# Performance work log

Hardware: AMD Instinct MI355X
Metric: run time of the kernel (lower is better)

Reference implementation:

```python
import jax, jax.numpy as jnp
from jax import lax
import numpy as np

B, N, F = 256, 131072, 16


def _fir(x, h):
    """y[i] = x[i] + sum_{j=0}^{F-1} h[j] * x[i-j-1] for i >= F, else 0.

    x: (B, N) float, h: (F,) float. Implemented as one causal conv with an
    effective (F+1)-tap kernel k where k[0] = 1 (identity) and k[1:] = h.
    """
    f = h.shape[0]
    k = jnp.concatenate([jnp.ones((1,), dtype=h.dtype), h])          # (F+1,)
    # XLA conv is cross-correlation: out[i] = sum_d rhs[d] * lhs_pad[i+d].
    # With left-pad f and a reversed kernel, out[i] = sum_d k[d] * x[i-d].
    out = lax.conv_general_dilated(
        x[:, None, :],                        # (B, 1, N)
        k[::-1][None, None, :],               # (1, 1, F+1)
        window_strides=(1,),
        padding=[(f, 0)],
        dimension_numbers=("NCH", "OIH", "NCH"),
    )[:, 0, :]                                # (B, N)
    # Original code leaves y[i] = 0 for i < F.
    mask = jnp.arange(x.shape[-1]) >= f       # (N,)
    return jnp.where(mask, out, jnp.zeros((), dtype=x.dtype))


def setup_inputs() -> dict:
    key = jax.random.key(0)
    k1, k2 = jax.random.split(key)
    x = jax.random.normal(k1, (B, N), dtype=jnp.float32)
    # keras 'random_normal' initializer: stddev = 0.05
    kernel = jax.random.normal(k2, (1, F), dtype=jnp.float32) * 0.05
    return {"x": x, "kernel": kernel}


def reference(x, kernel):
    h = kernel[0]              # (F,) forward taps
    hr = h[::-1]               # reversed kernel (self.kernel_r)
    v = _fir(x, h)             # first deconv pass with kernel
    y = _fir(v, hr)            # second deconv pass with reversed kernel
    return y
```

## Files before the change

### kernel.cpp

```cpp
#include <hip/hip_runtime.h>


#define NROW 131072
#define TILE 4096
#define HALO 32
#define PADIDX(j) ((j) + ((((j) >> 5)) << 2))
#define LDS_FLOATS (PADIDX(TILE + HALO - 1) + 1)

typedef float f32x4 __attribute__((ext_vector_type(4)));

__global__ void compute_g_kernel(const float* __restrict__ h, float* __restrict__ g) {
    int m = threadIdx.x;
    if (m < 33) {
        float s = 0.f;
#pragma unroll
        for (int a = 0; a <= 16; ++a) {
            int b = m - a;
            if (b >= 0 && b <= 16) {
                float ka = (a == 0) ? 1.f : h[a - 1];
                float kb = (b == 0) ? 1.f : h[16 - b];
                s += ka * kb;
            }
        }
        g[m] = s;
    }
}

__global__ __launch_bounds__(256) void fir2_kernel(const float* __restrict__ x,
                                                   const float* __restrict__ g,
                                                   const float* __restrict__ h,
                                                   float* __restrict__ y) {
    __shared__ __align__(16) float lds[LDS_FLOATS];

    const int bid = blockIdx.x;
    const int row = bid >> 5;
    const int chunk = bid & 31;
    const int i0 = chunk * TILE;
    const int t = (int)threadIdx.x;
    const float* __restrict__ xr = x + (size_t)row * NROW;
    float* __restrict__ yr = y + (size_t)row * NROW;

    float gg[33];
#pragma unroll
    for (int m = 0; m < 33; ++m) gg[m] = g[m];

    const int base = i0 - HALO;
#pragma unroll
    for (int k = 0; k < 4; ++k) {
        const int f = t + 256 * k;
        const int gidx = base + 4 * f;
        f32x4 v = (f32x4)(0.f);
        if (gidx >= 0) v = *(const f32x4*)(xr + gidx);
        *(f32x4*)(lds + PADIDX(4 * f)) = v;
    }
    if (t < 8) {
        const int f = 1024 + t;
        f32x4 v = *(const f32x4*)(xr + base + 4 * f);
        *(f32x4*)(lds + PADIDX(4 * f)) = v;
    }
    __syncthreads();

#pragma unroll 1
    for (int k = 0; k < 4; ++k) {
        const int jb = 1024 * k + 4 * t;
        float w[36];
#pragma unroll
        for (int q = 0; q < 9; ++q) {
            const f32x4 v = *(const f32x4*)(lds + PADIDX(jb + 4 * q));
            w[4 * q + 0] = v.x; w[4 * q + 1] = v.y;
            w[4 * q + 2] = v.z; w[4 * q + 3] = v.w;
        }
        f32x4 o;
#pragma unroll
        for (int c = 0; c < 4; ++c) {
            float s = 0.f;
#pragma unroll
            for (int m = 0; m < 33; ++m) s = fmaf(gg[m], w[c + 32 - m], s);
            o[c] = s;
        }
        __builtin_nontemporal_store(o, (f32x4*)(yr + i0 + jb));
    }

    if (chunk == 0 && t < 8) {
        f32x4 o = (f32x4)(0.f);
        if (t >= 4) {
            float hh[16];
#pragma unroll
            for (int j = 0; j < 16; ++j) hh[j] = h[j];
            float vloc[16];
#pragma unroll
            for (int u = 0; u < 16; ++u) {
                const int p = 16 + u;
                float s = lds[PADIDX(p + 32)];
#pragma unroll
                for (int j = 0; j < 16; ++j)
                    s = fmaf(hh[j], lds[PADIDX(p + 31 - j)], s);
                vloc[u] = s;
            }
#pragma unroll
            for (int p = 16; p < 32; ++p) {
                float s = vloc[p - 16];
#pragma unroll
                for (int j = 0; j < 16; ++j)
                    if (j <= p - 17) s = fmaf(hh[15 - j], vloc[p - 17 - j], s);
                if ((p >> 2) == t) o[p & 3] = s;
            }
        }
        __builtin_nontemporal_store(o, (f32x4*)(yr + 4 * t));
    }
}

extern "C" void kernel_launch(void* const* d_in, const int* in_sizes, int n_in,
                              void* d_out, int out_size, void* d_ws, size_t ws_size,
                              hipStream_t stream) {
    const float* x = (const float*)d_in[0];
    const float* h = (const float*)d_in[1];
    float* y = (float*)d_out;
    float* g = (float*)d_ws;
    (void)in_sizes; (void)n_in; (void)out_size; (void)ws_size;

    compute_g_kernel<<<1, 64, 0, stream>>>(h, g);
    fir2_kernel<<<8192, 256, 0, stream>>>(x, g, h, y);
}
```

Baseline: 236.9 us.

## Drop LDS staging and read FIR windows directly from global memory

Removes the shared-memory tile and barrier. Each thread now loads its 36-sample window straight from global memory and computes one 4-output group. The grid grows fourfold so each block covers a quarter of the previous tile. Overlapping window reads now rely on L1/L2 caching instead of explicit LDS reuse, which trades extra global load traffic for no sync and no LDS occupancy limit.

```diff
diff --git a/kernel.cpp b/kernel.cpp
--- a/kernel.cpp
+++ b/kernel.cpp
@@ -2,10 +2,6 @@
 
 
 #define NROW 131072
-#define TILE 4096
-#define HALO 32
-#define PADIDX(j) ((j) + ((((j) >> 5)) << 2))
-#define LDS_FLOATS (PADIDX(TILE + HALO - 1) + 1)
 
 typedef float f32x4 __attribute__((ext_vector_type(4)));
 
@@ -30,13 +26,11 @@
                                                    const float* __restrict__ g,
                                                    const float* __restrict__ h,
                                                    float* __restrict__ y) {
-    __shared__ __align__(16) float lds[LDS_FLOATS];
-
     const int bid = blockIdx.x;
-    const int row = bid >> 5;
-    const int chunk = bid & 31;
-    const int i0 = chunk * TILE;
+    const int row = bid >> 7;
+    const int blk = bid & 127;
     const int t = (int)threadIdx.x;
+    const int p0 = (blk << 10) + 4 * t;
     const float* __restrict__ xr = x + (size_t)row * NROW;
     float* __restrict__ yr = y + (size_t)row * NROW;
 
@@ -44,45 +38,38 @@
 #pragma unroll
     for (int m = 0; m < 33; ++m) gg[m] = g[m];
 
-    const int base = i0 - HALO;
-#pragma unroll
-    for (int k = 0; k < 4; ++k) {
-        const int f = t + 256 * k;
-        const int gidx = base + 4 * f;
-        f32x4 v = (f32x4)(0.f);
-        if (gidx >= 0) v = *(const f32x4*)(xr + gidx);
-        *(f32x4*)(lds + PADIDX(4 * f)) = v;
-    }
-    if (t < 8) {
-        const int f = 1024 + t;
-        f32x4 v = *(const f32x4*)(xr + base + 4 * f);
-        *(f32x4*)(lds + PADIDX(4 * f)) = v;
-    }
-    __syncthreads();
-
-#pragma unroll 1
-    for (int k = 0; k < 4; ++k) {
-        const int jb = 1024 * k + 4 * t;
-        float w[36];
+    float w[36];
+    const float* __restrict__ wp = xr + p0 - 32;
+    if (blk != 0) {
 #pragma unroll
         for (int q = 0; q < 9; ++q) {
-            const f32x4 v = *(const f32x4*)(lds + PADIDX(jb + 4 * q));
+            const f32x4 v = *(const f32x4*)(wp + 4 * q);
             w[4 * q + 0] = v.x; w[4 * q + 1] = v.y;
             w[4 * q + 2] = v.z; w[4 * q + 3] = v.w;
         }
-        f32x4 o;
+    } else {
 #pragma unroll
-        for (int c = 0; c < 4; ++c) {
-            float s = 0.f;
-#pragma unroll
-            for (int m = 0; m < 33; ++m) s = fmaf(gg[m], w[c + 32 - m], s);
-            o[c] = s;
+        for (int q = 0; q < 9; ++q) {
+            const int gidx = p0 - 32 + 4 * q;
+            f32x4 v = (f32x4)(0.f);
+            if (gidx >= 0) v = *(const f32x4*)(xr + gidx);
+            w[4 * q + 0] = v.x; w[4 * q + 1] = v.y;
+            w[4 * q + 2] = v.z; w[4 * q + 3] = v.w;
         }
-        __builtin_nontemporal_store(o, (f32x4*)(yr + i0 + jb));
     }
 
-    if (chunk == 0 && t < 8) {
-        f32x4 o = (f32x4)(0.f);
+    f32x4 o;
+#pragma unroll
+    for (int c = 0; c < 4; ++c) {
+        float s = 0.f;
+#pragma unroll
+        for (int m = 0; m < 33; ++m) s = fmaf(gg[m], w[c + 32 - m], s);
+        o[c] = s;
+    }
+    __builtin_nontemporal_store(o, (f32x4*)(yr + p0));
+
+    if (blk == 0 && t < 8) {
+        f32x4 ofix = (f32x4)(0.f);
         if (t >= 4) {
             float hh[16];
 #pragma unroll
@@ -91,10 +78,10 @@
 #pragma unroll
             for (int u = 0; u < 16; ++u) {
                 const int p = 16 + u;
-                float s = lds[PADIDX(p + 32)];
+                float s = xr[p];
 #pragma unroll
                 for (int j = 0; j < 16; ++j)
-                    s = fmaf(hh[j], lds[PADIDX(p + 31 - j)], s);
+                    s = fmaf(hh[j], xr[p - 1 - j], s);
                 vloc[u] = s;
             }
 #pragma unroll
@@ -103,10 +90,10 @@
 #pragma unroll
                 for (int j = 0; j < 16; ++j)
                     if (j <= p - 17) s = fmaf(hh[15 - j], vloc[p - 17 - j], s);
-                if ((p >> 2) == t) o[p & 3] = s;
+                if ((p >> 2) == t) ofix[p & 3] = s;
             }
         }
-        __builtin_nontemporal_store(o, (f32x4*)(yr + 4 * t));
+        __builtin_nontemporal_store(ofix, (f32x4*)(yr + 4 * t));
     }
 }
 
@@ -120,5 +107,5 @@
     (void)in_sizes; (void)n_in; (void)out_size; (void)ws_size;
 
     compute_g_kernel<<<1, 64, 0, stream>>>(h, g);
-    fir2_kernel<<<8192, 256, 0, stream>>>(x, g, h, y);
+    fir2_kernel<<<32768, 256, 0, stream>>>(x, g, h, y);
 }
```

After: 253.2 us. +6.9%, slower.

## Give each wavefront its own LDS sub-tile and drop block-wide barrier

Applied to the files above, without the earlier changes.

Splits the 4096-element block tile into four 1024-element per-wavefront tiles, each with its own 32-element halo in LDS, so a wave only reads data it loaded. This replaces __syncthreads with a wave barrier and drops the padded LDS indexing, since each wave now works on a contiguous slice. It also hoists the zero-padding check so only the first wave of chunk 0 does it. The cost is extra halo loads (four per block instead of one) and possible LDS bank conflicts from the unpadded stride-4 vector reads.

```diff
diff --git a/kernel.cpp b/kernel.cpp
--- a/kernel.cpp
+++ b/kernel.cpp
@@ -3,9 +3,9 @@
 
 #define NROW 131072
 #define TILE 4096
+#define WTILE 1024
 #define HALO 32
-#define PADIDX(j) ((j) + ((((j) >> 5)) << 2))
-#define LDS_FLOATS (PADIDX(TILE + HALO - 1) + 1)
+#define WLDS (WTILE + HALO)
 
 typedef float f32x4 __attribute__((ext_vector_type(4)));
 
@@ -26,63 +26,80 @@
     }
 }
 
+__device__ __forceinline__ f32x4 conv4(const float (&w)[36], const float (&gg)[33]) {
+    f32x4 o;
+#pragma unroll
+    for (int c = 0; c < 4; ++c) {
+        float s = 0.f;
+#pragma unroll
+        for (int m = 0; m < 33; ++m) s = fmaf(gg[m], w[c + 32 - m], s);
+        o[c] = s;
+    }
+    return o;
+}
+
 __global__ __launch_bounds__(256) void fir2_kernel(const float* __restrict__ x,
                                                    const float* __restrict__ g,
                                                    const float* __restrict__ h,
                                                    float* __restrict__ y) {
-    __shared__ __align__(16) float lds[LDS_FLOATS];
+    __shared__ __align__(16) float lds[4 * WLDS];
 
     const int bid = blockIdx.x;
     const int row = bid >> 5;
     const int chunk = bid & 31;
-    const int i0 = chunk * TILE;
     const int t = (int)threadIdx.x;
+    const int wv = t >> 6;
+    const int l = t & 63;
+    const int i0w = chunk * TILE + wv * WTILE;
     const float* __restrict__ xr = x + (size_t)row * NROW;
     float* __restrict__ yr = y + (size_t)row * NROW;
+    float* const ldsw = lds + wv * WLDS;
 
     float gg[33];
 #pragma unroll
     for (int m = 0; m < 33; ++m) gg[m] = g[m];
 
-    const int base = i0 - HALO;
+    const int base = i0w - HALO;
+    if (chunk == 0 && wv == 0) {
 #pragma unroll
-    for (int k = 0; k < 4; ++k) {
-        const int f = t + 256 * k;
-        const int gidx = base + 4 * f;
-        f32x4 v = (f32x4)(0.f);
-        if (gidx >= 0) v = *(const f32x4*)(xr + gidx);
-        *(f32x4*)(lds + PADIDX(4 * f)) = v;
+        for (int k = 0; k < 4; ++k) {
+            const int f = l + 64 * k;
+            const int gidx = base + 4 * f;
+            f32x4 v = (f32x4)(0.f);
+            if (gidx >= 0) v = *(const f32x4*)(xr + gidx);
+            *(f32x4*)(ldsw + 4 * f) = v;
+        }
+    } else {
+#pragma unroll
+        for (int k = 0; k < 4; ++k) {
+            const int f = l + 64 * k;
+            f32x4 v = *(const f32x4*)(xr + base + 4 * f);
+            *(f32x4*)(ldsw + 4 * f) = v;
+        }
     }
-    if (t < 8) {
-        const int f = 1024 + t;
+    if (l < 8) {
+        const int f = 256 + l;
         f32x4 v = *(const f32x4*)(xr + base + 4 * f);
-        *(f32x4*)(lds + PADIDX(4 * f)) = v;
+        *(f32x4*)(ldsw + 4 * f) = v;
     }
-    __syncthreads();
+    __builtin_amdgcn_wave_barrier();
 
 #pragma unroll 1
     for (int k = 0; k < 4; ++k) {
-        const int jb = 1024 * k + 4 * t;
+        const int jb = 256 * k + 4 * l;
         float w[36];
 #pragma unroll
         for (int q = 0; q < 9; ++q) {
-            const f32x4 v = *(const f32x4*)(lds + PADIDX(jb + 4 * q));
+            const f32x4 v = *(const f32x4*)(ldsw + jb + 4 * q);
             w[4 * q + 0] = v.x; w[4 * q + 1] = v.y;
             w[4 * q + 2] = v.z; w[4 * q + 3] = v.w;
         }
-        f32x4 o;
-#pragma unroll
-        for (int c = 0; c < 4; ++c) {
-            float s = 0.f;
-#pragma unroll
-            for (int m = 0; m < 33; ++m) s = fmaf(gg[m], w[c + 32 - m], s);
-            o[c] = s;
-        }
-        __builtin_nontemporal_store(o, (f32x4*)(yr + i0 + jb));
+        const f32x4 o = conv4(w, gg);
+        __builtin_nontemporal_store(o, (f32x4*)(yr + i0w + jb));
     }
 
     if (chunk == 0 && t < 8) {
-        f32x4 o = (f32x4)(0.f);
+        f32x4 ofix = (f32x4)(0.f);
         if (t >= 4) {
             float hh[16];
 #pragma unroll
@@ -91,10 +108,10 @@
 #pragma unroll
             for (int u = 0; u < 16; ++u) {
                 const int p = 16 + u;
-                float s = lds[PADIDX(p + 32)];
+                float s = ldsw[p + 32];
 #pragma unroll
                 for (int j = 0; j < 16; ++j)
-                    s = fmaf(hh[j], lds[PADIDX(p + 31 - j)], s);
+                    s = fmaf(hh[j], ldsw[p + 31 - j], s);
                 vloc[u] = s;
             }
 #pragma unroll
@@ -103,10 +120,10 @@
 #pragma unroll
                 for (int j = 0; j < 16; ++j)
                     if (j <= p - 17) s = fmaf(hh[15 - j], vloc[p - 17 - j], s);
-                if ((p >> 2) == t) o[p & 3] = s;
+                if ((p >> 2) == t) ofix[p & 3] = s;
             }
         }
-        __builtin_nontemporal_store(o, (f32x4*)(yr + 4 * t));
+        __builtin_nontemporal_store(ofix, (f32x4*)(yr + 4 * t));
     }
 }
 
```

Measured after the change: 236.4 us. About the same (-0.2%).
